# Optimization experiments

Hardware: AMD Instinct MI355X
Metric: run time of the kernel (lower is better)

The kernel has to match this reference:

```python
import jax, jax.numpy as jnp
import numpy as np

BN_EPS = 1e-5


def setup_inputs() -> dict:
    key = jax.random.key(0)
    ks = jax.random.split(key, 6)
    N_IN, N_OUT, K3, P, C_IN, C_OUT = 100000, 200000, 27, 80000, 64, 64
    features = jax.random.normal(ks[0], (N_IN, C_IN), dtype=jnp.float32)
    weight = jax.random.normal(ks[1], (K3, C_IN, C_OUT), dtype=jnp.float32) * 0.05
    bias = jnp.zeros((C_OUT,), dtype=jnp.float32)
    gamma = jnp.ones((C_OUT,), dtype=jnp.float32)
    beta = jnp.zeros((C_OUT,), dtype=jnp.float32)
    pairs_in = jax.random.randint(ks[2], (K3, P), 0, N_IN, dtype=jnp.int32)
    pairs_out = jax.random.randint(ks[3], (K3, P), 0, N_OUT, dtype=jnp.int32)
    return {
        "features": features, "weight": weight, "bias": bias,
        "gamma": gamma, "beta": beta,
        "pairs_in": pairs_in, "pairs_out": pairs_out, "n_out": N_OUT,
    }


def reference(features, weight, bias, gamma, beta, pairs_in, pairs_out, n_out):
    # --- SparseInverseConv3d: gather -> per-offset GEMM -> scatter-add ---
    C_out = weight.shape[2]
    gathered = features[pairs_in]                      # [K3, P, C_in]
    prod = jnp.einsum('kpc,kcd->kpd', gathered, weight)  # [K3, P, C_out]
    out = jnp.zeros((n_out, C_out), dtype=features.dtype)
    out = out.at[pairs_out.reshape(-1)].add(prod.reshape(-1, C_out))
    out = out + bias                                   # [N_out, C_out]
    # --- BatchNorm1d (training mode: batch stats, biased var) ---
    mean = jnp.mean(out, axis=0)
    var = jnp.var(out, axis=0)
    y = (out - mean) * jax.lax.rsqrt(var + BN_EPS) * gamma + beta
    # --- ReLU ---
    return jnp.maximum(y, 0.0)
```

## Files before the change

kernel.cpp:

```cpp
#include <hip/hip_runtime.h>
#include <hip/hip_fp16.h>


#define C_DIM 64
#define LDS_STRIDE 72
#define ROW_STRIDE 68

typedef __bf16 bf16_t;
typedef bf16_t bf16x4 __attribute__((ext_vector_type(4)));
typedef bf16_t bf16x8 __attribute__((ext_vector_type(8)));
typedef float floatx4 __attribute__((ext_vector_type(4)));

__global__ __launch_bounds__(256)
void k_fprep(const float* __restrict__ f, bf16_t* __restrict__ fb, int total4)
{
    int i = blockIdx.x * 256 + threadIdx.x;
    if (i < total4) {
        float4 v = ((const float4*)f)[i];
        bf16x4 o;
        o[0] = (bf16_t)v.x; o[1] = (bf16_t)v.y;
        o[2] = (bf16_t)v.z; o[3] = (bf16_t)v.w;
        ((bf16x4*)fb)[i] = o;
    }
}

__global__ __launch_bounds__(256)
void k1_fp16(const float* __restrict__ features,
             const bf16_t* __restrict__ fbf16,
             const float* __restrict__ weight,
             const int* __restrict__ pairs_in,
             const int* __restrict__ pairs_out,
             __half* __restrict__ acc,
             int P, int rows_per_block, int use_bf16)
{
    __shared__ bf16_t Wt[C_DIM * LDS_STRIDE];
    __shared__ float  scratch[4][16 * ROW_STRIDE];

    const int k   = blockIdx.y;
    const int tid = threadIdx.x;

    const float* Wk = weight + (size_t)k * C_DIM * C_DIM;
    for (int i = tid; i < C_DIM * C_DIM; i += 256) {
        int c = i >> 6, d = i & 63;
        Wt[d * LDS_STRIDE + c] = (bf16_t)Wk[i];
    }
    __syncthreads();

    const int wave = tid >> 6;
    const int lane = tid & 63;
    const int quad = lane >> 4;
    const int col  = lane & 15;
    const int sub  = lane >> 5;
    const int c2   = lane & 31;
    float* ls = &scratch[wave][0];

    bf16x8 bfrag[2][4];
    #pragma unroll
    for (int ks = 0; ks < 2; ++ks)
        #pragma unroll
        for (int nt = 0; nt < 4; ++nt)
            bfrag[ks][nt] =
                *(const bf16x8*)&Wt[(col + 16 * nt) * LDS_STRIDE + quad * 8 + 32 * ks];

    const int* __restrict__ pin  = pairs_in  + (size_t)k * P;
    const int* __restrict__ pout = pairs_out + (size_t)k * P;

    const int p0   = blockIdx.x * rows_per_block;
    const int pend = min(p0 + rows_per_block, P);

    for (int base = p0 + wave * 16; base < pend; base += 64) {
        int prow    = base + col;
        int clamped = (prow < pend) ? prow : (pend - 1);
        int in_idx  = pin[clamped];
        int out_idx = pout[clamped];

        bf16x8 a0, a1;
        if (use_bf16) {
            const bf16_t* src = fbf16 + (size_t)in_idx * C_DIM + quad * 8;
            a0 = *(const bf16x8*)(src);
            a1 = *(const bf16x8*)(src + 32);
        } else {
            const float* src = features + (size_t)in_idx * C_DIM + quad * 8;
            float4 f0 = *(const float4*)(src);
            float4 f1 = *(const float4*)(src + 4);
            float4 f2 = *(const float4*)(src + 32);
            float4 f3 = *(const float4*)(src + 36);
            a0[0] = (bf16_t)f0.x; a0[1] = (bf16_t)f0.y; a0[2] = (bf16_t)f0.z; a0[3] = (bf16_t)f0.w;
            a0[4] = (bf16_t)f1.x; a0[5] = (bf16_t)f1.y; a0[6] = (bf16_t)f1.z; a0[7] = (bf16_t)f1.w;
            a1[0] = (bf16_t)f2.x; a1[1] = (bf16_t)f2.y; a1[2] = (bf16_t)f2.z; a1[3] = (bf16_t)f2.w;
            a1[4] = (bf16_t)f3.x; a1[5] = (bf16_t)f3.y; a1[6] = (bf16_t)f3.z; a1[7] = (bf16_t)f3.w;
        }

        floatx4 acc0 = {0.f, 0.f, 0.f, 0.f};
        floatx4 acc1 = {0.f, 0.f, 0.f, 0.f};
        floatx4 acc2 = {0.f, 0.f, 0.f, 0.f};
        floatx4 acc3 = {0.f, 0.f, 0.f, 0.f};

        acc0 = __builtin_amdgcn_mfma_f32_16x16x32_bf16(a0, bfrag[0][0], acc0, 0, 0, 0);
        acc0 = __builtin_amdgcn_mfma_f32_16x16x32_bf16(a1, bfrag[1][0], acc0, 0, 0, 0);
        acc1 = __builtin_amdgcn_mfma_f32_16x16x32_bf16(a0, bfrag[0][1], acc1, 0, 0, 0);
        acc1 = __builtin_amdgcn_mfma_f32_16x16x32_bf16(a1, bfrag[1][1], acc1, 0, 0, 0);
        acc2 = __builtin_amdgcn_mfma_f32_16x16x32_bf16(a0, bfrag[0][2], acc2, 0, 0, 0);
        acc2 = __builtin_amdgcn_mfma_f32_16x16x32_bf16(a1, bfrag[1][2], acc2, 0, 0, 0);
        acc3 = __builtin_amdgcn_mfma_f32_16x16x32_bf16(a0, bfrag[0][3], acc3, 0, 0, 0);
        acc3 = __builtin_amdgcn_mfma_f32_16x16x32_bf16(a1, bfrag[1][3], acc3, 0, 0, 0);

        #pragma unroll
        for (int r = 0; r < 4; ++r) {
            int m = quad * 4 + r;
            ls[m * ROW_STRIDE + col +  0] = acc0[r];
            ls[m * ROW_STRIDE + col + 16] = acc1[r];
            ls[m * ROW_STRIDE + col + 32] = acc2[r];
            ls[m * ROW_STRIDE + col + 48] = acc3[r];
        }
        asm volatile("s_waitcnt lgkmcnt(0)" ::: "memory");

        #pragma unroll
        for (int m2 = 0; m2 < 8; ++m2) {
            int m = m2 * 2 + sub;
            float2 v = *(const float2*)&ls[m * ROW_STRIDE + 2 * c2];
            __half2 h = __floats2half2_rn(v.x, v.y);
            int g = __shfl(out_idx, m);
            if (base + m < pend)
                unsafeAtomicAdd((__half2*)(acc + (size_t)g * C_DIM + 2 * c2), h);
        }
    }
}

__global__ __launch_bounds__(256)
void k2_stats_h(const __half* __restrict__ acc, float* __restrict__ sums,
                int n_rows)
{
    const int tid = threadIdx.x;
    const int c8  = tid & 7;
    const int sub = tid >> 3;

    float s[8] = {0,0,0,0,0,0,0,0}, q[8] = {0,0,0,0,0,0,0,0};
    for (int r = blockIdx.x * 32 + sub; r < n_rows; r += gridDim.x * 32) {
        float4 v = *(const float4*)&acc[(size_t)r * C_DIM + c8 * 8];
        const __half2* h = (const __half2*)&v;
        #pragma unroll
        for (int j = 0; j < 4; ++j) {
            float x = __half2float(h[j].x), y = __half2float(h[j].y);
            s[2*j]   += x; q[2*j]   += x * x;
            s[2*j+1] += y; q[2*j+1] += y * y;
        }
    }

    __shared__ float red[128];
    if (tid < 128) red[tid] = 0.f;
    __syncthreads();
    #pragma unroll
    for (int j = 0; j < 8; ++j) {
        atomicAdd(&red[c8 * 8 + j], s[j]);
        atomicAdd(&red[64 + c8 * 8 + j], q[j]);
    }
    __syncthreads();
    if (tid < 128) atomicAdd(&sums[tid], red[tid]);
}

__global__ __launch_bounds__(256)
void k3_bn_relu_h(const __half* __restrict__ acc, float* __restrict__ out,
                  const float* __restrict__ sums,
                  const float* __restrict__ gamma, const float* __restrict__ beta,
                  int n_rows)
{
    int tid = blockIdx.x * 256 + threadIdx.x;
    int c8  = tid & 7;
    float inv_n = 1.0f / (float)n_rows;

    float sc[8], sh[8];
    #pragma unroll
    for (int j = 0; j < 8; ++j) {
        int ch    = c8 * 8 + j;
        float m   = sums[ch] * inv_n;
        float var = sums[64 + ch] * inv_n - m * m;
        float inv = rsqrtf(var + 1e-5f);
        float g   = gamma[ch] * inv;
        sc[j] = g;
        sh[j] = beta[ch] - m * g;
    }

    size_t total = (size_t)n_rows * 8;
    for (size_t i = tid; i < total; i += (size_t)gridDim.x * 256) {
        float4 v = ((const float4*)acc)[i];
        const __half2* h = (const __half2*)&v;
        float4 o0, o1;
        o0.x = fmaxf(__half2float(h[0].x) * sc[0] + sh[0], 0.f);
        o0.y = fmaxf(__half2float(h[0].y) * sc[1] + sh[1], 0.f);
        o0.z = fmaxf(__half2float(h[1].x) * sc[2] + sh[2], 0.f);
        o0.w = fmaxf(__half2float(h[1].y) * sc[3] + sh[3], 0.f);
        o1.x = fmaxf(__half2float(h[2].x) * sc[4] + sh[4], 0.f);
        o1.y = fmaxf(__half2float(h[2].y) * sc[5] + sh[5], 0.f);
        o1.z = fmaxf(__half2float(h[3].x) * sc[6] + sh[6], 0.f);
        o1.w = fmaxf(__half2float(h[3].y) * sc[7] + sh[7], 0.f);
        ((float4*)out)[2 * i]     = o0;
        ((float4*)out)[2 * i + 1] = o1;
    }
}

__global__ __launch_bounds__(256)
void k1_scatter_gemm(const float* __restrict__ features,
                     const float* __restrict__ weight,
                     const int* __restrict__ pairs_in,
                     const int* __restrict__ pairs_out,
                     float* __restrict__ out,
                     int P, int rows_per_block)
{
    __shared__ bf16_t Wt[C_DIM * LDS_STRIDE];
    const int k   = blockIdx.y;
    const int tid = threadIdx.x;
    const float* Wk = weight + (size_t)k * C_DIM * C_DIM;
    for (int i = tid; i < C_DIM * C_DIM; i += 256) {
        int c = i >> 6, d = i & 63;
        Wt[d * LDS_STRIDE + c] = (bf16_t)Wk[i];
    }
    __syncthreads();
    const int wave = tid >> 6, lane = tid & 63, quad = lane >> 4, col = lane & 15;
    bf16x8 bfrag[2][4];
    #pragma unroll
    for (int ks = 0; ks < 2; ++ks)
        #pragma unroll
        for (int nt = 0; nt < 4; ++nt)
            bfrag[ks][nt] =
                *(const bf16x8*)&Wt[(col + 16 * nt) * LDS_STRIDE + quad * 8 + 32 * ks];
    const int* __restrict__ pin  = pairs_in  + (size_t)k * P;
    const int* __restrict__ pout = pairs_out + (size_t)k * P;
    const int p0   = blockIdx.x * rows_per_block;
    const int pend = min(p0 + rows_per_block, P);
    for (int base = p0 + wave * 16; base < pend; base += 64) {
        int prow    = base + col;
        int clamped = (prow < pend) ? prow : (pend - 1);
        int in_idx  = pin[clamped];
        int out_idx = pout[clamped];
        const float* src = features + (size_t)in_idx * C_DIM + quad * 8;
        float4 f0 = *(const float4*)(src);
        float4 f1 = *(const float4*)(src + 4);
        float4 f2 = *(const float4*)(src + 32);
        float4 f3 = *(const float4*)(src + 36);
        bf16x8 a0, a1;
        a0[0] = (bf16_t)f0.x; a0[1] = (bf16_t)f0.y; a0[2] = (bf16_t)f0.z; a0[3] = (bf16_t)f0.w;
        a0[4] = (bf16_t)f1.x; a0[5] = (bf16_t)f1.y; a0[6] = (bf16_t)f1.z; a0[7] = (bf16_t)f1.w;
        a1[0] = (bf16_t)f2.x; a1[1] = (bf16_t)f2.y; a1[2] = (bf16_t)f2.z; a1[3] = (bf16_t)f2.w;
        a1[4] = (bf16_t)f3.x; a1[5] = (bf16_t)f3.y; a1[6] = (bf16_t)f3.z; a1[7] = (bf16_t)f3.w;
        floatx4 acc0 = {0.f,0.f,0.f,0.f}, acc1 = {0.f,0.f,0.f,0.f};
        floatx4 acc2 = {0.f,0.f,0.f,0.f}, acc3 = {0.f,0.f,0.f,0.f};
        acc0 = __builtin_amdgcn_mfma_f32_16x16x32_bf16(a0, bfrag[0][0], acc0, 0, 0, 0);
        acc0 = __builtin_amdgcn_mfma_f32_16x16x32_bf16(a1, bfrag[1][0], acc0, 0, 0, 0);
        acc1 = __builtin_amdgcn_mfma_f32_16x16x32_bf16(a0, bfrag[0][1], acc1, 0, 0, 0);
        acc1 = __builtin_amdgcn_mfma_f32_16x16x32_bf16(a1, bfrag[1][1], acc1, 0, 0, 0);
        acc2 = __builtin_amdgcn_mfma_f32_16x16x32_bf16(a0, bfrag[0][2], acc2, 0, 0, 0);
        acc2 = __builtin_amdgcn_mfma_f32_16x16x32_bf16(a1, bfrag[1][2], acc2, 0, 0, 0);
        acc3 = __builtin_amdgcn_mfma_f32_16x16x32_bf16(a0, bfrag[0][3], acc3, 0, 0, 0);
        acc3 = __builtin_amdgcn_mfma_f32_16x16x32_bf16(a1, bfrag[1][3], acc3, 0, 0, 0);
        #pragma unroll
        for (int r = 0; r < 4; ++r) {
            int m = quad * 4 + r;
            int g = __shfl(out_idx, m);
            if (base + m < pend) {
                float* dst = out + (size_t)g * C_DIM + col;
                unsafeAtomicAdd(dst +  0, acc0[r]);
                unsafeAtomicAdd(dst + 16, acc1[r]);
                unsafeAtomicAdd(dst + 32, acc2[r]);
                unsafeAtomicAdd(dst + 48, acc3[r]);
            }
        }
    }
}

__global__ __launch_bounds__(256)
void k2_stats(const float* __restrict__ acc, float* __restrict__ sums, int n_rows)
{
    int tid = threadIdx.x;
    int ch  = tid & 63;
    int sub = tid >> 6;
    float s = 0.f, s2 = 0.f;
    for (int r = blockIdx.x * 4 + sub; r < n_rows; r += gridDim.x * 4) {
        float v = acc[(size_t)r * C_DIM + ch];
        s  += v;
        s2 += v * v;
    }
    __shared__ float red[256];
    red[tid] = s;
    __syncthreads();
    if (tid < 64) {
        float t = red[tid] + red[tid + 64] + red[tid + 128] + red[tid + 192];
        atomicAdd(&sums[ch], t);
    }
    __syncthreads();
    red[tid] = s2;
    __syncthreads();
    if (tid < 64) {
        float t = red[tid] + red[tid + 64] + red[tid + 128] + red[tid + 192];
        atomicAdd(&sums[64 + ch], t);
    }
}

__global__ __launch_bounds__(256)
void k3_bn_relu(float* __restrict__ out, const float* __restrict__ sums,
                const float* __restrict__ gamma, const float* __restrict__ beta,
                int n_rows)
{
    int tid = blockIdx.x * 256 + threadIdx.x;
    int ch0 = (tid * 4) & 63;
    float inv_n = 1.0f / (float)n_rows;
    float sc[4], sh[4];
    #pragma unroll
    for (int j = 0; j < 4; ++j) {
        int ch    = ch0 + j;
        float m   = sums[ch] * inv_n;
        float var = sums[64 + ch] * inv_n - m * m;
        float inv = rsqrtf(var + 1e-5f);
        float g   = gamma[ch] * inv;
        sc[j] = g;
        sh[j] = beta[ch] - m * g;
    }
    size_t total = (size_t)n_rows * C_DIM / 4;
    for (size_t i = tid; i < total; i += (size_t)gridDim.x * 256) {
        float4 v = ((const float4*)out)[i];
        v.x = fmaxf(v.x * sc[0] + sh[0], 0.f);
        v.y = fmaxf(v.y * sc[1] + sh[1], 0.f);
        v.z = fmaxf(v.z * sc[2] + sh[2], 0.f);
        v.w = fmaxf(v.w * sc[3] + sh[3], 0.f);
        ((float4*)out)[i] = v;
    }
}

extern "C" void kernel_launch(void* const* d_in, const int* in_sizes, int n_in,
                              void* d_out, int out_size, void* d_ws, size_t ws_size,
                              hipStream_t stream)
{
    const float* features  = (const float*)d_in[0];
    const float* weight    = (const float*)d_in[1];
    const float* gamma     = (const float*)d_in[3];
    const float* beta      = (const float*)d_in[4];
    const int*   pairs_in  = (const int*)d_in[5];
    const int*   pairs_out = (const int*)d_in[6];

    const int n_out     = out_size / C_DIM;
    const int n_in_rows = in_sizes[0] / C_DIM;
    const int K3        = in_sizes[1] / (C_DIM * C_DIM);
    const int P         = in_sizes[5] / K3;

    float* out = (float*)d_out;

    size_t acc_bytes = (size_t)n_out * C_DIM * 2;
    size_t off_acc   = 512;
    size_t off_fb    = (off_acc + acc_bytes + 255) & ~(size_t)255;
    size_t fb_bytes  = (size_t)n_in_rows * C_DIM * 2;
    size_t need_b    = off_acc + acc_bytes;
    size_t need_a    = off_fb + fb_bytes;

    float*  sums  = (float*)d_ws;
    __half* acc   = (__half*)((char*)d_ws + off_acc);
    bf16_t* fbf16 = (bf16_t*)((char*)d_ws + off_fb);

    const int rows_per_block = 512;
    dim3 g1((P + rows_per_block - 1) / rows_per_block, K3);

    if (ws_size >= need_b) {
        const int use_bf16 = (ws_size >= need_a) ? 1 : 0;

        hipMemsetAsync(d_ws, 0, off_acc + acc_bytes, stream);
        if (use_bf16)
            k_fprep<<<(n_in_rows * 16 + 255) / 256, 256, 0, stream>>>(
                features, fbf16, n_in_rows * 16);

        k1_fp16<<<g1, 256, 0, stream>>>(features, fbf16, weight, pairs_in,
                                        pairs_out, acc, P, rows_per_block,
                                        use_bf16);

        k2_stats_h<<<dim3(256), 256, 0, stream>>>(acc, sums, n_out);
        k3_bn_relu_h<<<dim3(512), 256, 0, stream>>>(acc, out, sums, gamma,
                                                    beta, n_out);
    } else {
        hipMemsetAsync(d_out, 0, (size_t)out_size * sizeof(float), stream);
        hipMemsetAsync(d_ws, 0, 512, stream);

        k1_scatter_gemm<<<g1, 256, 0, stream>>>(features, weight, pairs_in,
                                                pairs_out, out, P, rows_per_block);
        k2_stats<<<dim3(1024), 256, 0, stream>>>(out, sums, n_out);
        k3_bn_relu<<<dim3(1024), 256, 0, stream>>>(out, sums, gamma, beta, n_out);
    }
}
```

Before: 357.2 us.

## Fuse zero-init into prep kernel and merge stats with BN-ReLU via grid barrier

The memset of the sums header and fp16 accumulator now happens inside the bf16 feature-conversion kernel, so one launch replaces a memset plus a kernel. The stats and BN/ReLU kernels are merged into one persistent kernel of 512 blocks that syncs through an atomic ticket spin barrier before normalizing. This cuts launch overhead and lets later reads of acc hit cache. The barrier assumes all 512 blocks are resident at once, which risks deadlock if they are not.

```diff
diff --git a/kernel.cpp b/kernel.cpp
--- a/kernel.cpp
+++ b/kernel.cpp
@@ -12,16 +12,22 @@
 typedef float floatx4 __attribute__((ext_vector_type(4)));
 
 __global__ __launch_bounds__(256)
-void k_fprep(const float* __restrict__ f, bf16_t* __restrict__ fb, int total4)
+void k_prep(const float* __restrict__ f, bf16_t* __restrict__ fb,
+            float4* __restrict__ accz, float* __restrict__ hdr,
+            int total4, int accz4)
 {
     int i = blockIdx.x * 256 + threadIdx.x;
-    if (i < total4) {
-        float4 v = ((const float4*)f)[i];
+    int stride = gridDim.x * 256;
+    if (i < 136) hdr[i] = 0.f;
+    for (int j = i; j < total4; j += stride) {
+        float4 v = ((const float4*)f)[j];
         bf16x4 o;
         o[0] = (bf16_t)v.x; o[1] = (bf16_t)v.y;
         o[2] = (bf16_t)v.z; o[3] = (bf16_t)v.w;
-        ((bf16x4*)fb)[i] = o;
-    }
+        ((bf16x4*)fb)[j] = o;
+    }
+    float4 z = {0.f, 0.f, 0.f, 0.f};
+    for (int j = i; j < accz4; j += stride) accz[j] = z;
 }
 
 __global__ __launch_bounds__(256)
@@ -124,6 +130,82 @@
             if (base + m < pend)
                 unsafeAtomicAdd((__half2*)(acc + (size_t)g * C_DIM + 2 * c2), h);
         }
+    }
+}
+
+__global__ __launch_bounds__(256)
+void k23_fused(const __half* __restrict__ acc, float* __restrict__ out,
+               float* __restrict__ sums, int* __restrict__ ticket,
+               const float* __restrict__ gamma, const float* __restrict__ beta,
+               int n_rows, int nblocks)
+{
+    const int tid = threadIdx.x;
+    const int c8  = tid & 7;
+    const int sub = tid >> 3;
+
+    float s[8] = {0,0,0,0,0,0,0,0}, q[8] = {0,0,0,0,0,0,0,0};
+    for (int r = blockIdx.x * 32 + sub; r < n_rows; r += nblocks * 32) {
+        float4 v = *(const float4*)&acc[(size_t)r * C_DIM + c8 * 8];
+        const __half2* h = (const __half2*)&v;
+        #pragma unroll
+        for (int j = 0; j < 4; ++j) {
+            float x = __half2float(h[j].x), y = __half2float(h[j].y);
+            s[2*j]   += x; q[2*j]   += x * x;
+            s[2*j+1] += y; q[2*j+1] += y * y;
+        }
+    }
+    __shared__ float red[128];
+    if (tid < 128) red[tid] = 0.f;
+    __syncthreads();
+    #pragma unroll
+    for (int j = 0; j < 8; ++j) {
+        atomicAdd(&red[c8 * 8 + j], s[j]);
+        atomicAdd(&red[64 + c8 * 8 + j], q[j]);
+    }
+    __syncthreads();
+    if (tid < 128) unsafeAtomicAdd(&sums[tid], red[tid]);
+    __syncthreads();
+
+    if (tid == 0) {
+        __threadfence();
+        atomicAdd(ticket, 1);
+        while (atomicAdd(ticket, 0) < nblocks)
+            __builtin_amdgcn_s_sleep(1);
+    }
+    __syncthreads();
+
+    __shared__ float snap[128];
+    if (tid < 128) snap[tid] = unsafeAtomicAdd(&sums[tid], 0.0f);
+    __syncthreads();
+
+    float inv_n = 1.0f / (float)n_rows;
+    float sc[8], sh[8];
+    #pragma unroll
+    for (int j = 0; j < 8; ++j) {
+        int ch    = c8 * 8 + j;
+        float m   = snap[ch] * inv_n;
+        float var = snap[64 + ch] * inv_n - m * m;
+        float inv = rsqrtf(var + 1e-5f);
+        float g   = gamma[ch] * inv;
+        sc[j] = g;
+        sh[j] = beta[ch] - m * g;
+    }
+
+    size_t total = (size_t)n_rows * 8;
+    for (size_t i = blockIdx.x * 256 + tid; i < total; i += (size_t)nblocks * 256) {
+        float4 v = ((const float4*)acc)[i];
+        const __half2* h = (const __half2*)&v;
+        float4 o0, o1;
+        o0.x = fmaxf(__half2float(h[0].x) * sc[0] + sh[0], 0.f);
+        o0.y = fmaxf(__half2float(h[0].y) * sc[1] + sh[1], 0.f);
+        o0.z = fmaxf(__half2float(h[1].x) * sc[2] + sh[2], 0.f);
+        o0.w = fmaxf(__half2float(h[1].y) * sc[3] + sh[3], 0.f);
+        o1.x = fmaxf(__half2float(h[2].x) * sc[4] + sh[4], 0.f);
+        o1.y = fmaxf(__half2float(h[2].y) * sc[5] + sh[5], 0.f);
+        o1.z = fmaxf(__half2float(h[3].x) * sc[6] + sh[6], 0.f);
+        o1.w = fmaxf(__half2float(h[3].y) * sc[7] + sh[7], 0.f);
+        ((float4*)out)[2 * i]     = o0;
+        ((float4*)out)[2 * i + 1] = o1;
     }
 }
 
@@ -344,32 +426,36 @@
 
     float* out = (float*)d_out;
 
+    const size_t off_acc = 1024;
     size_t acc_bytes = (size_t)n_out * C_DIM * 2;
-    size_t off_acc   = 512;
     size_t off_fb    = (off_acc + acc_bytes + 255) & ~(size_t)255;
     size_t fb_bytes  = (size_t)n_in_rows * C_DIM * 2;
     size_t need_b    = off_acc + acc_bytes;
     size_t need_a    = off_fb + fb_bytes;
 
-    float*  sums  = (float*)d_ws;
-    __half* acc   = (__half*)((char*)d_ws + off_acc);
-    bf16_t* fbf16 = (bf16_t*)((char*)d_ws + off_fb);
+    float*  sums   = (float*)d_ws;
+    int*    ticket = (int*)((char*)d_ws + 512);
+    __half* acc    = (__half*)((char*)d_ws + off_acc);
+    bf16_t* fbf16  = (bf16_t*)((char*)d_ws + off_fb);
 
     const int rows_per_block = 512;
     dim3 g1((P + rows_per_block - 1) / rows_per_block, K3);
 
-    if (ws_size >= need_b) {
-        const int use_bf16 = (ws_size >= need_a) ? 1 : 0;
-
+    if (ws_size >= need_a) {
+        k_prep<<<dim3(2048), 256, 0, stream>>>(features, fbf16,
+                                               (float4*)acc, (float*)d_ws,
+                                               n_in_rows * 16,
+                                               (int)(acc_bytes / 16));
+
+        k1_fp16<<<g1, 256, 0, stream>>>(features, fbf16, weight, pairs_in,
+                                        pairs_out, acc, P, rows_per_block, 1);
+
+        k23_fused<<<dim3(512), 256, 0, stream>>>(acc, out, sums, ticket,
+                                                 gamma, beta, n_out, 512);
+    } else if (ws_size >= need_b) {
         hipMemsetAsync(d_ws, 0, off_acc + acc_bytes, stream);
-        if (use_bf16)
-            k_fprep<<<(n_in_rows * 16 + 255) / 256, 256, 0, stream>>>(
-                features, fbf16, n_in_rows * 16);
-
         k1_fp16<<<g1, 256, 0, stream>>>(features, fbf16, weight, pairs_in,
-                                        pairs_out, acc, P, rows_per_block,
-                                        use_bf16);
-
+                                        pairs_out, acc, P, rows_per_block, 0);
         k2_stats_h<<<dim3(256), 256, 0, stream>>>(acc, sums, n_out);
         k3_bn_relu_h<<<dim3(512), 256, 0, stream>>>(acc, out, sums, gamma,
                                                     beta, n_out);
```

Result: slower. 387.7 us (+8.5%).
